# Performance work log

Hardware: AMD Instinct MI355X
Metric: run time of the kernel (lower is better)

Reference implementation:

```python
import jax, jax.numpy as jnp
import numpy as np

D_MODEL = 1024
D_INTERNAL = 256


def setup_inputs() -> dict:
    key = jax.random.key(0)
    ks = jax.random.split(key, 10)
    s = lambda fan_in: 1.0 / np.sqrt(fan_in)
    inp = {
        "input_vecs": jax.random.normal(ks[0], (4, 2048, D_MODEL), dtype=jnp.float32),
        # Linear weights stored as (in, out) for x @ W
        "wq": jax.random.uniform(ks[1], (D_MODEL, D_INTERNAL), minval=-s(D_MODEL), maxval=s(D_MODEL), dtype=jnp.float32),
        "wk": jax.random.uniform(ks[2], (D_MODEL, D_INTERNAL), minval=-s(D_MODEL), maxval=s(D_MODEL), dtype=jnp.float32),
        "wv": jax.random.uniform(ks[3], (D_MODEL, D_MODEL), minval=-s(D_MODEL), maxval=s(D_MODEL), dtype=jnp.float32),
        "wo": jax.random.uniform(ks[4], (D_MODEL, D_MODEL), minval=-s(D_MODEL), maxval=s(D_MODEL), dtype=jnp.float32),
        "bo": jax.random.uniform(ks[5], (D_MODEL,), minval=-s(D_MODEL), maxval=s(D_MODEL), dtype=jnp.float32),
        "w1": jax.random.uniform(ks[6], (D_MODEL, D_INTERNAL), minval=-s(D_MODEL), maxval=s(D_MODEL), dtype=jnp.float32),
        "b1": jax.random.uniform(ks[7], (D_INTERNAL,), minval=-s(D_MODEL), maxval=s(D_MODEL), dtype=jnp.float32),
        "w2": jax.random.uniform(ks[8], (D_INTERNAL, D_MODEL), minval=-s(D_INTERNAL), maxval=s(D_INTERNAL), dtype=jnp.float32),
        "b2": jax.random.uniform(ks[9], (D_MODEL,), minval=-s(D_INTERNAL), maxval=s(D_INTERNAL), dtype=jnp.float32),
    }
    return inp


def reference(input_vecs, wq, wk, wv, wo, bo, w1, b1, w2, b2):
    # Single-head self-attention (causal=False default path)
    q = jnp.einsum("btd,dk->btk", input_vecs, wq)  # (B,T,d_internal)
    k = jnp.einsum("btd,dk->btk", input_vecs, wk)
    v = jnp.einsum("btd,de->bte", input_vecs, wv)  # (B,T,d_model)
    scale = 1.0 / jnp.sqrt(jnp.asarray(q.shape[-1], dtype=q.dtype))
    scores = jnp.einsum("bqk,btk->bqt", q, k) * scale  # (B,T,T)
    attn = jax.nn.softmax(scores, axis=-1)
    context = jnp.einsum("bqt,bte->bqe", attn, v)  # (B,T,d_model)
    context = jnp.einsum("bte,eo->bto", context, wo) + bo
    residual = input_vecs + context
    h = jax.nn.relu(jnp.einsum("btd,dk->btk", residual, w1) + b1)
    ff = jnp.einsum("btk,kd->btd", h, w2) + b2
    out = residual + ff
    return out, attn
```

## Files before the change

kernel.cpp:

```cpp
#include <hip/hip_runtime.h>

typedef unsigned short u16;
typedef unsigned int u32;
typedef __bf16 bf16x8 __attribute__((ext_vector_type(8)));
typedef float f32x4 __attribute__((ext_vector_type(4)));

#define MTOT 8192
#define DM 1024
#define DI 256
#define TT 2048

__device__ __forceinline__ u16 f2bf(float f) {
    u32 u = __float_as_uint(f);
    return (u16)((u + 0x7fffu + ((u >> 16) & 1u)) >> 16);
}
__device__ __forceinline__ float b2f(u16 b) {
    return __uint_as_float((u32)b << 16);
}

__device__ __forceinline__ void transpose_tile(const float* __restrict__ in,
                                               u16* __restrict__ out, int K, int N,
                                               int bx, int by) {
    __shared__ float t[32][33];
    int n0 = bx * 32, k0 = by * 32;
    int tx = threadIdx.x & 31, ty = threadIdx.x >> 5;
    #pragma unroll
    for (int i = ty; i < 32; i += 8) t[i][tx] = in[(long)(k0 + i) * N + n0 + tx];
    __syncthreads();
    #pragma unroll
    for (int i = ty; i < 32; i += 8) out[(long)(n0 + i) * K + k0 + tx] = f2bf(t[tx][i]);
}

__device__ __forceinline__ void cvt_range(const float* __restrict__ in,
                                          u16* __restrict__ out, long n4, int b, int nb) {
    long i = (long)b * 256 + threadIdx.x;
    long stride = (long)nb * 256;
    for (; i < n4; i += stride) {
        float4 v = reinterpret_cast<const float4*>(in)[i];
        union { u16 u[4]; uint2 p; } o;
        o.u[0] = f2bf(v.x); o.u[1] = f2bf(v.y); o.u[2] = f2bf(v.z); o.u[3] = f2bf(v.w);
        reinterpret_cast<uint2*>(out)[i] = o.p;
    }
}

__global__ __launch_bounds__(256) void prep_kernel(
    const float* __restrict__ x, u16* __restrict__ Xb,
    const float* __restrict__ wq, const float* __restrict__ wk, u16* __restrict__ Wqk_t,
    const float* __restrict__ wv, u16* __restrict__ Wv_b,
    const float* __restrict__ wo, u16* __restrict__ Wo_t,
    const float* __restrict__ w1, u16* __restrict__ W1_t,
    const float* __restrict__ w2, u16* __restrict__ W2_t)
{
    int b = blockIdx.x;
    if (b < 1024) { cvt_range(x, Xb, (long)MTOT * DM / 4, b, 1024); return; }
    b -= 1024;
    if (b < 256)  { transpose_tile(wq, Wqk_t,              1024,  256, b & 7,  b >> 3); return; }
    b -= 256;
    if (b < 256)  { transpose_tile(wk, Wqk_t + 256 * 1024, 1024,  256, b & 7,  b >> 3); return; }
    b -= 256;
    if (b < 256)  { cvt_range(wv, Wv_b, (long)DM * DM / 4, b, 256); return; }
    b -= 256;
    if (b < 1024) { transpose_tile(wo, Wo_t,               1024, 1024, b & 31, b >> 5); return; }
    b -= 1024;
    if (b < 256)  { transpose_tile(w1, W1_t,               1024,  256, b & 7,  b >> 3); return; }
    b -= 256;
    transpose_tile(w2, W2_t, 256, 1024, b & 31, b >> 5);
}

__global__ __launch_bounds__(256) void softmax_kernel(u16* __restrict__ Sb, float* __restrict__ attn) {
    long row = blockIdx.x;
    int tid = threadIdx.x;
    uint4 q = reinterpret_cast<uint4*>(Sb + row * (long)TT)[tid];
    u32 w4[4] = {q.x, q.y, q.z, q.w};
    float vv[8];
    #pragma unroll
    for (int j = 0; j < 4; ++j) {
        vv[2 * j]     = __uint_as_float(w4[j] << 16);
        vv[2 * j + 1] = __uint_as_float(w4[j] & 0xffff0000u);
    }
    float m = vv[0];
    #pragma unroll
    for (int j = 1; j < 8; ++j) m = fmaxf(m, vv[j]);
    #pragma unroll
    for (int off = 32; off; off >>= 1) m = fmaxf(m, __shfl_xor(m, off));
    __shared__ float redm[4], reds[4];
    if ((tid & 63) == 0) redm[tid >> 6] = m;
    __syncthreads();
    m = fmaxf(fmaxf(redm[0], redm[1]), fmaxf(redm[2], redm[3]));
    float s = 0.f;
    #pragma unroll
    for (int j = 0; j < 8; ++j) { vv[j] = __expf(vv[j] - m); s += vv[j]; }
    #pragma unroll
    for (int off = 32; off; off >>= 1) s += __shfl_xor(s, off);
    if ((tid & 63) == 0) reds[tid >> 6] = s;
    __syncthreads();
    s = reds[0] + reds[1] + reds[2] + reds[3];
    float inv = 1.0f / s;
    #pragma unroll
    for (int j = 0; j < 8; ++j) vv[j] *= inv;
    float* p = attn + row * (long)TT;
    reinterpret_cast<float4*>(p)[tid * 2]     = make_float4(vv[0], vv[1], vv[2], vv[3]);
    reinterpret_cast<float4*>(p)[tid * 2 + 1] = make_float4(vv[4], vv[5], vv[6], vv[7]);
    union { u16 u[8]; uint4 q; } pk;
    #pragma unroll
    for (int j = 0; j < 8; ++j) pk.u[j] = f2bf(vv[j]);
    reinterpret_cast<uint4*>(Sb + row * (long)TT)[tid] = pk.q;
}

template<int MODE>
__device__ __forceinline__ void gemm_body(
    u16* As, u16* Bs,
    const u16* __restrict__ A, int lda,
    const u16* __restrict__ Bt, int ldb,
    u16* __restrict__ Cb, int ldcb,
    float* __restrict__ Cf, int ldcf,
    int K, float scale,
    const float* __restrict__ bias,
    const u16* __restrict__ addend_b, int ld_add,
    long tile_m, long tile_n)
{
    const int tid = threadIdx.x;
    const int w = tid >> 6;
    const int l = tid & 63;
    const int lane15 = l & 15;
    const int lhi = l >> 4;

    const int srow = w * 8 + (l >> 3);
    const int scol = (((l & 7) ^ (l >> 3)) << 4) >> 1;

    const u16* aptr = A + (tile_m + srow) * (long)lda + scol;
    const u16* bptr = Bt + (tile_n + srow) * (long)ldb + scol;

    f32x4 acc[4][4] = {};

    const int wr = (w >> 1) * 64;
    const int wc = (w & 1) * 64;

    for (int k0 = 0; k0 < K; k0 += 64) {
        #pragma unroll
        for (int i = 0; i < 4; ++i) {
            __builtin_amdgcn_global_load_lds(
                (const __attribute__((address_space(1))) void*)(aptr + (long)i * 32 * lda + k0),
                (__attribute__((address_space(3))) void*)((char*)As + i * 4096 + w * 1024),
                16, 0, 0);
        }
        #pragma unroll
        for (int i = 0; i < 4; ++i) {
            __builtin_amdgcn_global_load_lds(
                (const __attribute__((address_space(1))) void*)(bptr + (long)i * 32 * ldb + k0),
                (__attribute__((address_space(3))) void*)((char*)Bs + i * 4096 + w * 1024),
                16, 0, 0);
        }
        __syncthreads();
        #pragma unroll
        for (int kk = 0; kk < 2; ++kk) {
            bf16x8 af[4], bfr[4];
            const int kb = (kk * 32 + lhi * 8) * 2;
            #pragma unroll
            for (int m = 0; m < 4; ++m) {
                int r = wr + m * 16 + lane15;
                af[m] = *reinterpret_cast<const bf16x8*>(
                    (const char*)As + r * 128 + (kb ^ ((r & 7) << 4)));
            }
            #pragma unroll
            for (int n = 0; n < 4; ++n) {
                int r = wc + n * 16 + lane15;
                bfr[n] = *reinterpret_cast<const bf16x8*>(
                    (const char*)Bs + r * 128 + (kb ^ ((r & 7) << 4)));
            }
            #pragma unroll
            for (int m = 0; m < 4; ++m)
                #pragma unroll
                for (int n = 0; n < 4; ++n)
                    acc[m][n] = __builtin_amdgcn_mfma_f32_16x16x32_bf16(
                        af[m], bfr[n], acc[m][n], 0, 0, 0);
        }
        __syncthreads();
    }

    #pragma unroll
    for (int m = 0; m < 4; ++m) {
        #pragma unroll
        for (int n = 0; n < 4; ++n) {
            long grow0 = tile_m + wr + m * 16 + lhi * 4;
            long gcol  = tile_n + wc + n * 16 + lane15;
            #pragma unroll
            for (int r = 0; r < 4; ++r) {
                long grow = grow0 + r;
                float v = acc[m][n][r];
                if (MODE == 0) v *= scale;
                if (MODE == 3 || MODE == 6 || MODE == 7) v += bias[gcol];
                if (MODE == 6 || MODE == 7) v += b2f(addend_b[grow * (long)ld_add + gcol]);
                if (MODE == 3) v = fmaxf(v, 0.0f);
                if (MODE == 0 || MODE == 3 || MODE == 6) Cb[grow * (long)ldcb + gcol] = f2bf(v);
                if (MODE == 1) Cb[gcol * (long)ldcb + grow] = f2bf(v);
                if (MODE == 7) Cf[grow * (long)ldcf + gcol] = v;
            }
        }
    }
}

__device__ __forceinline__ int xcd_swizzle(int bid, int nb) {
    return (bid & 7) * (nb >> 3) + (bid >> 3);
}

template<int MODE>
__global__ __launch_bounds__(256) void gemm_bt(
    const u16* __restrict__ A, long sA, int lda,
    const u16* __restrict__ Bt, long sB, int ldb,
    u16* __restrict__ Cb, long sCb, int ldcb,
    float* __restrict__ Cf, long sCf, int ldcf,
    int K, float scale,
    const float* __restrict__ bias,
    const u16* __restrict__ addend_b, long sAdd, int ld_add,
    int gx, int gy)
{
    __shared__ __attribute__((aligned(16))) u16 As[128 * 64];
    __shared__ __attribute__((aligned(16))) u16 Bs[128 * 64];

    int lid = xcd_swizzle(blockIdx.x, gridDim.x);
    int x = lid % gx;
    int t = lid / gx;
    int y = t % gy;
    int z = t / gy;

    gemm_body<MODE>(As, Bs,
                    A + (long)z * sA, lda, Bt + (long)z * sB, ldb,
                    Cb + (long)z * sCb, ldcb, Cf + (long)z * sCf, ldcf,
                    K, scale, bias,
                    addend_b ? addend_b + (long)z * sAdd : addend_b, ld_add,
                    (long)y * 128, (long)x * 128);
}

__global__ __launch_bounds__(256) void gemm_qkv(
    const u16* __restrict__ Xb, const u16* __restrict__ Wqk_t, u16* __restrict__ QKb,
    const u16* __restrict__ Wvo_t, u16* __restrict__ VWt)
{
    __shared__ __attribute__((aligned(16))) u16 As[128 * 64];
    __shared__ __attribute__((aligned(16))) u16 Bs[128 * 64];

    int lid = xcd_swizzle(blockIdx.x, gridDim.x);
    if (lid < 256) {
        int x = lid & 3, y = lid >> 2;
        gemm_body<0>(As, Bs, Xb, 1024, Wqk_t, 1024, QKb, 512,
                     (float*)nullptr, 0, 1024, 1.0f,
                     (const float*)nullptr, (const u16*)nullptr, 0,
                     (long)y * 128, (long)x * 128);
    } else {
        int l2 = lid - 256;
        int x = l2 & 7, y = l2 >> 3;
        gemm_body<1>(As, Bs, Xb, 1024, Wvo_t, 1024, VWt, 8192,
                     (float*)nullptr, 0, 1024, 1.0f,
                     (const float*)nullptr, (const u16*)nullptr, 0,
                     (long)y * 128, (long)x * 128);
    }
}

extern "C" void kernel_launch(void* const* d_in, const int* in_sizes, int n_in,
                              void* d_out, int out_size, void* d_ws, size_t ws_size,
                              hipStream_t stream)
{
    const float* x  = (const float*)d_in[0];
    const float* wq = (const float*)d_in[1];
    const float* wk = (const float*)d_in[2];
    const float* wv = (const float*)d_in[3];
    const float* wo = (const float*)d_in[4];
    const float* bo = (const float*)d_in[5];
    const float* w1 = (const float*)d_in[6];
    const float* b1 = (const float*)d_in[7];
    const float* w2 = (const float*)d_in[8];
    const float* b2 = (const float*)d_in[9];

    float* out_f  = (float*)d_out;
    float* attn_f = out_f + (long)MTOT * DM;

    char* ws = (char*)d_ws;
    u16* Xb    = (u16*)(ws + 0);
    u16* Wqk_t = (u16*)(ws + 16777216);
    u16* Wv_b  = (u16*)(ws + 17825792);
    u16* Wo_t  = (u16*)(ws + 19922944);
    u16* W1_t  = (u16*)(ws + 22020096);
    u16* W2_t  = (u16*)(ws + 22544384);
    u16* Wvo_t = (u16*)(ws + 23068672);
    u16* QKb   = (u16*)(ws + 25165824);
    u16* VWt   = (u16*)(ws + 33554432);
    u16* attnb = (u16*)(ws + 50331648);
    u16* res_b = (u16*)(ws + 83886080);
    u16* hb    = QKb;

    dim3 blk(256);

    prep_kernel<<<dim3(3328), blk, 0, stream>>>(x, Xb, wq, wk, Wqk_t, wv, Wv_b,
                                                wo, Wo_t, w1, W1_t, w2, W2_t);
    gemm_bt<1><<<dim3(64), blk, 0, stream>>>(
        Wv_b, 0L, 1024, Wo_t, 0L, 1024, Wvo_t, 0L, 1024,
        (float*)nullptr, 0L, 0, 1024, 1.0f, (const float*)nullptr,
        (const u16*)nullptr, 0L, 0, 8, 8);
    gemm_qkv<<<dim3(768), blk, 0, stream>>>(Xb, Wqk_t, QKb, Wvo_t, VWt);
    gemm_bt<0><<<dim3(1024), blk, 0, stream>>>(
        QKb, (long)2048 * 512, 512, QKb + 256, (long)2048 * 512, 512,
        attnb, (long)2048 * 2048, 2048, (float*)nullptr, 0L, 0,
        256, 0.0625f, (const float*)nullptr, (const u16*)nullptr, 0L, 0, 16, 16);
    softmax_kernel<<<dim3(8192), blk, 0, stream>>>(attnb, attn_f);
    gemm_bt<6><<<dim3(512), blk, 0, stream>>>(
        attnb, (long)2048 * 2048, 2048, VWt, 2048L, 8192,
        res_b, (long)2048 * 1024, 1024, (float*)nullptr, 0L, 0,
        2048, 1.0f, bo, Xb, (long)2048 * 1024, 1024, 8, 16);
    gemm_bt<3><<<dim3(128), blk, 0, stream>>>(
        res_b, 0L, 1024, W1_t, 0L, 1024, hb, 0L, 256,
        (float*)nullptr, 0L, 0, 1024, 1.0f, b1, (const u16*)nullptr, 0L, 0, 2, 64);
    gemm_bt<7><<<dim3(512), blk, 0, stream>>>(
        hb, 0L, 256, W2_t, 0L, 256, (u16*)nullptr, 0L, 0,
        out_f, 0L, 1024, 256, 1.0f, b2, res_b, 0L, 1024, 8, 64);
}
```

Baseline: 197.7 us.

## Add 256x256 double-buffered 8-wave GEMM for QKV, scores and context

Introduces a 512-thread GEMM body with 256x256 output tiles, a double-buffered LDS pipeline that prefetches the next K tile during MFMA work, and s_setprio around the MFMA blocks. The QKV projection, the QK^T score GEMM and the attention-times-V GEMM use it, which raises per-block data reuse and hides global load latency. The V projection is now written by swapping the operands (Wvo_t as A, X as B) instead of storing transposed. Grids shrink to 192/256/128 blocks, which may underfill the 256 CUs, and 128KB of LDS allows only one block per CU.

```diff
diff --git a/kernel.cpp b/kernel.cpp
--- a/kernel.cpp
+++ b/kernel.cpp
@@ -9,6 +9,9 @@
 #define DM 1024
 #define DI 256
 #define TT 2048
+
+#define AS1 __attribute__((address_space(1)))
+#define AS3 __attribute__((address_space(3)))
 
 __device__ __forceinline__ u16 f2bf(float f) {
     u32 u = __float_as_uint(f);
@@ -107,6 +110,10 @@
     reinterpret_cast<uint4*>(Sb + row * (long)TT)[tid] = pk.q;
 }
 
+__device__ __forceinline__ int xcd_swizzle(int bid, int nb) {
+    return (bid & 7) * (nb >> 3) + (bid >> 3);
+}
+
 template<int MODE>
 __device__ __forceinline__ void gemm_body(
     u16* As, u16* Bs,
@@ -140,16 +147,14 @@
         #pragma unroll
         for (int i = 0; i < 4; ++i) {
             __builtin_amdgcn_global_load_lds(
-                (const __attribute__((address_space(1))) void*)(aptr + (long)i * 32 * lda + k0),
-                (__attribute__((address_space(3))) void*)((char*)As + i * 4096 + w * 1024),
-                16, 0, 0);
+                (const AS1 void*)(aptr + (long)i * 32 * lda + k0),
+                (AS3 void*)((char*)As + i * 4096 + w * 1024), 16, 0, 0);
         }
         #pragma unroll
         for (int i = 0; i < 4; ++i) {
             __builtin_amdgcn_global_load_lds(
-                (const __attribute__((address_space(1))) void*)(bptr + (long)i * 32 * ldb + k0),
-                (__attribute__((address_space(3))) void*)((char*)Bs + i * 4096 + w * 1024),
-                16, 0, 0);
+                (const AS1 void*)(bptr + (long)i * 32 * ldb + k0),
+                (AS3 void*)((char*)Bs + i * 4096 + w * 1024), 16, 0, 0);
         }
         __syncthreads();
         #pragma unroll
@@ -200,10 +205,6 @@
     }
 }
 
-__device__ __forceinline__ int xcd_swizzle(int bid, int nb) {
-    return (bid & 7) * (nb >> 3) + (bid >> 3);
-}
-
 template<int MODE>
 __global__ __launch_bounds__(256) void gemm_bt(
     const u16* __restrict__ A, long sA, int lda,
@@ -232,27 +233,160 @@
                     (long)y * 128, (long)x * 128);
 }
 
-__global__ __launch_bounds__(256) void gemm_qkv(
+template<int MODE>
+__device__ __forceinline__ void gemm256_body(
+    char* ldsb,
+    const u16* __restrict__ A, int lda,
+    const u16* __restrict__ Bt, int ldb,
+    u16* __restrict__ Cb, int ldcb,
+    float* __restrict__ Cf, int ldcf,
+    int K, float scale,
+    const float* __restrict__ bias,
+    const u16* __restrict__ addend_b, int ld_add,
+    long tile_m, long tile_n)
+{
+    const int tid = threadIdx.x;
+    const int w = tid >> 6;
+    const int l = tid & 63;
+    const int wm = w >> 2;
+    const int wn = w & 3;
+    const int lane15 = l & 15;
+    const int lhi = l >> 4;
+    const int sw = (l & 7) << 4;
+
+    const int srow = w * 8 + (l >> 3);
+    const int scol = ((l & 7) ^ (l >> 3)) * 8;
+    const u16* aS = A + (tile_m + srow) * (long)lda + scol;
+    const u16* bS = Bt + (tile_n + srow) * (long)ldb + scol;
+
+    auto STAGE = [&](int tile, int bufi) {
+        long kof = (long)tile << 6;
+        char* ab = ldsb + bufi * 65536;
+        #pragma unroll
+        for (int h = 0; h < 2; ++h)
+            #pragma unroll
+            for (int i = 0; i < 2; ++i) {
+                __builtin_amdgcn_global_load_lds(
+                    (const AS1 void*)(aS + (long)(h * 128 + i * 64) * lda + kof),
+                    (AS3 void*)(ab + h * 16384 + i * 8192 + w * 1024), 16, 0, 0);
+                __builtin_amdgcn_global_load_lds(
+                    (const AS1 void*)(bS + (long)(h * 128 + i * 64) * ldb + kof),
+                    (AS3 void*)(ab + 32768 + h * 16384 + i * 8192 + w * 1024), 16, 0, 0);
+            }
+    };
+
+    f32x4 acc[8][4] = {};
+
+    const int NT = K >> 6;
+    STAGE(0, 0);
+    STAGE(1, 1);
+    asm volatile("s_waitcnt vmcnt(8)" ::: "memory");
+    __builtin_amdgcn_s_barrier();
+
+    for (int u = 0; u < (NT >> 1); ++u) {
+        #pragma unroll
+        for (int half = 0; half < 2; ++half) {
+            const char* abuf = ldsb + half * 65536 + wm * 16384;
+            const char* bbuf = ldsb + half * 65536 + 32768 + (wn >> 1) * 16384;
+            #pragma unroll
+            for (int q = 0; q < 4; ++q) {
+                bf16x8 af[4][2], bfr[2][2];
+                #pragma unroll
+                for (int m = 0; m < 4; ++m) {
+                    int r = (q & 1) * 64 + m * 16 + lane15;
+                    #pragma unroll
+                    for (int ks = 0; ks < 2; ++ks)
+                        af[m][ks] = *reinterpret_cast<const bf16x8*>(
+                            abuf + r * 128 + ((ks * 64 + lhi * 16) ^ sw));
+                }
+                #pragma unroll
+                for (int n = 0; n < 2; ++n) {
+                    int rb = (wn & 1) * 64 + ((q >> 1) * 2 + n) * 16 + lane15;
+                    #pragma unroll
+                    for (int ks = 0; ks < 2; ++ks)
+                        bfr[n][ks] = *reinterpret_cast<const bf16x8*>(
+                            bbuf + rb * 128 + ((ks * 64 + lhi * 16) ^ sw));
+                }
+                if (half == 0 && q == 0 && u > 0) STAGE(2 * u + 1, 1);
+                if (half == 1 && q == 0 && 2 * u + 2 < NT) STAGE(2 * u + 2, 0);
+                __builtin_amdgcn_s_barrier();
+                __builtin_amdgcn_s_setprio(1);
+                #pragma unroll
+                for (int m = 0; m < 4; ++m)
+                    #pragma unroll
+                    for (int n = 0; n < 2; ++n)
+                        #pragma unroll
+                        for (int ks = 0; ks < 2; ++ks)
+                            acc[(q & 1) * 4 + m][(q >> 1) * 2 + n] =
+                                __builtin_amdgcn_mfma_f32_16x16x32_bf16(
+                                    af[m][ks], bfr[n][ks],
+                                    acc[(q & 1) * 4 + m][(q >> 1) * 2 + n], 0, 0, 0);
+                __builtin_amdgcn_s_setprio(0);
+                if (q == 3) asm volatile("s_waitcnt vmcnt(0)" ::: "memory");
+                __builtin_amdgcn_s_barrier();
+            }
+        }
+    }
+
+    #pragma unroll
+    for (int mf = 0; mf < 8; ++mf) {
+        #pragma unroll
+        for (int nf = 0; nf < 4; ++nf) {
+            long grow0 = tile_m + wm * 128 + mf * 16 + lhi * 4;
+            long gcol  = tile_n + wn * 64 + nf * 16 + lane15;
+            #pragma unroll
+            for (int r = 0; r < 4; ++r) {
+                long grow = grow0 + r;
+                float v = acc[mf][nf][r];
+                if (MODE == 0) v *= scale;
+                if (MODE == 6) v += bias[gcol] + b2f(addend_b[grow * (long)ld_add + gcol]);
+                if (MODE == 0 || MODE == 6) Cb[grow * (long)ldcb + gcol] = f2bf(v);
+            }
+        }
+    }
+}
+
+template<int MODE>
+__global__ __launch_bounds__(512) void gemm256_bt(
+    const u16* __restrict__ A, long sA, int lda,
+    const u16* __restrict__ Bt, long sB, int ldb,
+    u16* __restrict__ Cb, long sCb, int ldcb,
+    int K, float scale,
+    const float* __restrict__ bias,
+    const u16* __restrict__ addend_b, long sAdd, int ld_add,
+    int gx, int tpz)
+{
+    __shared__ __attribute__((aligned(16))) u16 lds[65536];
+    int lid = xcd_swizzle(blockIdx.x, gridDim.x);
+    int z = lid / tpz, rem = lid % tpz;
+    int x = rem % gx, y = rem / gx;
+    gemm256_body<MODE>((char*)lds,
+                       A + (long)z * sA, lda, Bt + (long)z * sB, ldb,
+                       Cb + (long)z * sCb, ldcb, (float*)nullptr, 0,
+                       K, scale, bias,
+                       addend_b ? addend_b + (long)z * sAdd : addend_b, ld_add,
+                       (long)y * 256, (long)x * 256);
+}
+
+__global__ __launch_bounds__(512) void gemm256_qkv(
     const u16* __restrict__ Xb, const u16* __restrict__ Wqk_t, u16* __restrict__ QKb,
     const u16* __restrict__ Wvo_t, u16* __restrict__ VWt)
 {
-    __shared__ __attribute__((aligned(16))) u16 As[128 * 64];
-    __shared__ __attribute__((aligned(16))) u16 Bs[128 * 64];
-
+    __shared__ __attribute__((aligned(16))) u16 lds[65536];
     int lid = xcd_swizzle(blockIdx.x, gridDim.x);
-    if (lid < 256) {
-        int x = lid & 3, y = lid >> 2;
-        gemm_body<0>(As, Bs, Xb, 1024, Wqk_t, 1024, QKb, 512,
-                     (float*)nullptr, 0, 1024, 1.0f,
-                     (const float*)nullptr, (const u16*)nullptr, 0,
-                     (long)y * 128, (long)x * 128);
+    if (lid < 64) {
+        int x = lid & 1, y = lid >> 1;
+        gemm256_body<0>((char*)lds, Xb, 1024, Wqk_t, 1024, QKb, 512,
+                        (float*)nullptr, 0, 1024, 1.0f,
+                        (const float*)nullptr, (const u16*)nullptr, 0,
+                        (long)y * 256, (long)x * 256);
     } else {
-        int l2 = lid - 256;
-        int x = l2 & 7, y = l2 >> 3;
-        gemm_body<1>(As, Bs, Xb, 1024, Wvo_t, 1024, VWt, 8192,
-                     (float*)nullptr, 0, 1024, 1.0f,
-                     (const float*)nullptr, (const u16*)nullptr, 0,
-                     (long)y * 128, (long)x * 128);
+        int l2 = lid - 64;
+        int x = l2 >> 2, y = l2 & 3;
+        gemm256_body<0>((char*)lds, Wvo_t, 1024, Xb, 1024, VWt, 8192,
+                        (float*)nullptr, 0, 1024, 1.0f,
+                        (const float*)nullptr, (const u16*)nullptr, 0,
+                        (long)y * 256, (long)x * 256);
     }
 }
 
@@ -288,7 +422,7 @@
     u16* res_b = (u16*)(ws + 83886080);
     u16* hb    = QKb;
 
-    dim3 blk(256);
+    dim3 blk(256), blk5(512);
 
     prep_kernel<<<dim3(3328), blk, 0, stream>>>(x, Xb, wq, wk, Wqk_t, wv, Wv_b,
                                                 wo, Wo_t, w1, W1_t, w2, W2_t);
@@ -296,16 +430,16 @@
         Wv_b, 0L, 1024, Wo_t, 0L, 1024, Wvo_t, 0L, 1024,
         (float*)nullptr, 0L, 0, 1024, 1.0f, (const float*)nullptr,
         (const u16*)nullptr, 0L, 0, 8, 8);
-    gemm_qkv<<<dim3(768), blk, 0, stream>>>(Xb, Wqk_t, QKb, Wvo_t, VWt);
-    gemm_bt<0><<<dim3(1024), blk, 0, stream>>>(
+    gemm256_qkv<<<dim3(192), blk5, 0, stream>>>(Xb, Wqk_t, QKb, Wvo_t, VWt);
+    gemm256_bt<0><<<dim3(256), blk5, 0, stream>>>(
         QKb, (long)2048 * 512, 512, QKb + 256, (long)2048 * 512, 512,
-        attnb, (long)2048 * 2048, 2048, (float*)nullptr, 0L, 0,
-        256, 0.0625f, (const float*)nullptr, (const u16*)nullptr, 0L, 0, 16, 16);
+        attnb, (long)2048 * 2048, 2048,
+        256, 0.0625f, (const float*)nullptr, (const u16*)nullptr, 0L, 0, 8, 64);
     softmax_kernel<<<dim3(8192), blk, 0, stream>>>(attnb, attn_f);
-    gemm_bt<6><<<dim3(512), blk, 0, stream>>>(
+    gemm256_bt<6><<<dim3(128), blk5, 0, stream>>>(
         attnb, (long)2048 * 2048, 2048, VWt, 2048L, 8192,
-        res_b, (long)2048 * 1024, 1024, (float*)nullptr, 0L, 0,
-        2048, 1.0f, bo, Xb, (long)2048 * 1024, 1024, 8, 16);
+        res_b, (long)2048 * 1024, 1024,
+        2048, 1.0f, bo, Xb, (long)2048 * 1024, 1024, 4, 32);
     gemm_bt<3><<<dim3(128), blk, 0, stream>>>(
         res_b, 0L, 1024, W1_t, 0L, 1024, hb, 0L, 256,
         (float*)nullptr, 0L, 0, 1024, 1.0f, b1, (const u16*)nullptr, 0L, 0, 2, 64);
```

New measurement: 225.5 us. 1.14x slower.
